# Performance work log

Measured on AMD Instinct MI355X. Metric: run time of the kernel, lower is better.

The kernel has to match this reference:

```python
import jax, jax.numpy as jnp
import numpy as np

N_EMBD = 768
HEAD_SIZE = 72
SEQ_LEN = 512
BATCH = 64

def setup_inputs() -> dict:
    key = jax.random.key(0)
    kx, kk, kq, kv = jax.random.split(key, 4)
    # Linear weights stored as [in, out] for x @ W; torch Linear init ~ U(-1/sqrt(in), 1/sqrt(in))
    bound = 1.0 / np.sqrt(N_EMBD)
    x = jax.random.normal(kx, (BATCH, SEQ_LEN, N_EMBD), dtype=jnp.float32)
    Wk = jax.random.uniform(kk, (N_EMBD, HEAD_SIZE), minval=-bound, maxval=bound, dtype=jnp.float32)
    Wq = jax.random.uniform(kq, (N_EMBD, HEAD_SIZE), minval=-bound, maxval=bound, dtype=jnp.float32)
    Wv = jax.random.uniform(kv, (N_EMBD, HEAD_SIZE), minval=-bound, maxval=bound, dtype=jnp.float32)
    return {"x": x, "Wk": Wk, "Wq": Wq, "Wv": Wv}

def reference(x, Wk, Wq, Wv):
    # Single causal self-attention head (dropout in eval mode = identity).
    k = x @ Wk  # [B, T, H]
    q = x @ Wq  # [B, T, H]
    v = x @ Wv  # [B, T, H]
    scale = k.shape[-1] ** (-0.5)
    scores = jnp.einsum('bth,bsh->bts', q, k) * scale  # [B, T, T]
    T = scores.shape[-1]
    causal = jnp.tril(jnp.ones((T, T), dtype=bool))
    scores = jnp.where(causal, scores, -jnp.inf)
    attn = jax.nn.softmax(scores, axis=-1)
    out = jnp.einsum('bts,bsh->bth', attn, v)  # [B, T, H]
    return out
```

## Files before the change

kernel.cpp:

```cpp
#include <hip/hip_runtime.h>


typedef short bf16x8 __attribute__((ext_vector_type(8)));
typedef float f32x4 __attribute__((ext_vector_type(4)));

#define DEVI __device__ __forceinline__

DEVI unsigned short f2bf(float f) {
  unsigned int u = __builtin_bit_cast(unsigned int, f);
  u = (u + 0x7fffu + ((u >> 16) & 1u)) >> 16;
  return (unsigned short)u;
}

DEVI void async16(void* lds, const void* g) {
  __builtin_amdgcn_global_load_lds(
      (const __attribute__((address_space(1))) unsigned int*)g,
      (__attribute__((address_space(3))) unsigned int*)lds, 16, 0, 0);
}

__global__ __launch_bounds__(256) void cast_x_k(const float* __restrict__ x,
                                                unsigned short* __restrict__ xb) {
  size_t i = ((size_t)blockIdx.x * 256 + threadIdx.x) * 8;
  float4 a = *(const float4*)(x + i);
  float4 c = *(const float4*)(x + i + 4);
  uint4 o;
  o.x = (unsigned)f2bf(a.x) | ((unsigned)f2bf(a.y) << 16);
  o.y = (unsigned)f2bf(a.z) | ((unsigned)f2bf(a.w) << 16);
  o.z = (unsigned)f2bf(c.x) | ((unsigned)f2bf(c.y) << 16);
  o.w = (unsigned)f2bf(c.z) | ((unsigned)f2bf(c.w) << 16);
  *(uint4*)(xb + i) = o;
}

__global__ __launch_bounds__(128) void cast_w_k(const float* __restrict__ Wk,
                                                const float* __restrict__ Wq,
                                                const float* __restrict__ Wv,
                                                unsigned short* __restrict__ wbt) {
  int mat = blockIdx.x / 80, h = blockIdx.x % 80;
  const float* W = (mat == 0) ? Wk : (mat == 1) ? Wq : Wv;
  float sc = (mat == 1) ? 0.11785113019775793f : 1.0f;
  for (int k = threadIdx.x; k < 768; k += 128) {
    float v = (h < 72) ? W[k * 72 + h] * sc : 0.0f;
    wbt[((size_t)mat * 80 + h) * 768 + k] = f2bf(v);
  }
}

struct ProjSmem {
  union {
    struct { short x[256 * 64]; short w[80 * 72]; } s;
    short t[80 * 264];
  };
};

__global__ __launch_bounds__(256, 2) void proj_k(
    const unsigned short* __restrict__ xb, const unsigned short* __restrict__ wbt,
    unsigned short* __restrict__ Kg, unsigned short* __restrict__ Qg,
    unsigned short* __restrict__ Vt) {
  __shared__ __align__(16) ProjSmem sm;
  const int mat = blockIdx.y;
  const int row0 = blockIdx.x * 256;
  const int tid = threadIdx.x, wave = tid >> 6, lane = tid & 63;
  const int quad = lane >> 4, l16 = lane & 15;

  f32x4 acc[4][5] = {};

  for (int k0 = 0; k0 < 768; k0 += 64) {
    for (int j = 0; j < 8; ++j) {
      int inst = wave * 8 + j;
      int r = inst * 8 + (lane >> 3);
      const unsigned short* g = xb + (size_t)(row0 + r) * 768 + k0 + (lane & 7) * 8;
      async16(&sm.s.x[inst * 512], g);
    }
    for (int c = tid; c < 640; c += 256) {
      int r = c >> 3, cc = (c & 7) * 8;
      uint4 d = *(const uint4*)(wbt + ((size_t)mat * 80 + r) * 768 + k0 + cc);
      *(uint4*)&sm.s.w[r * 72 + cc] = d;
    }
    __syncthreads();
    for (int ks = 0; ks < 2; ++ks) {
      bf16x8 af[4], bfr[5];
      for (int mt = 0; mt < 4; ++mt)
        af[mt] = *(const bf16x8*)&sm.s.x[(wave * 64 + mt * 16 + l16) * 64 + ks * 32 + quad * 8];
      for (int nt = 0; nt < 5; ++nt)
        bfr[nt] = *(const bf16x8*)&sm.s.w[(nt * 16 + l16) * 72 + ks * 32 + quad * 8];
      for (int mt = 0; mt < 4; ++mt)
        for (int nt = 0; nt < 5; ++nt)
          acc[mt][nt] = __builtin_amdgcn_mfma_f32_16x16x32_bf16(af[mt], bfr[nt], acc[mt][nt], 0, 0, 0);
    }
    __syncthreads();
  }

  if (mat < 2) {
    unsigned short* G = (mat == 0) ? Kg : Qg;
    for (int mt = 0; mt < 4; ++mt)
      for (int r = 0; r < 4; ++r) {
        size_t row = (size_t)row0 + wave * 64 + mt * 16 + quad * 4 + r;
        for (int nt = 0; nt < 5; ++nt)
          G[row * 96 + nt * 16 + l16] = f2bf(acc[mt][nt][r]);
        G[row * 96 + 80 + l16] = 0;
      }
  } else {
    for (int mt = 0; mt < 4; ++mt)
      for (int nt = 0; nt < 5; ++nt)
        for (int r = 0; r < 4; ++r)
          sm.t[(nt * 16 + l16) * 264 + wave * 64 + mt * 16 + quad * 4 + r] =
              (short)f2bf(acc[mt][nt][r]);
    __syncthreads();
    int b = blockIdx.x >> 1, t0 = (blockIdx.x & 1) * 256;
    for (int c = tid; c < 2560; c += 256) {
      int hr = c >> 5, tc = (c & 31) * 8;
      uint4 d = *(const uint4*)&sm.t[hr * 264 + tc];
      *(uint4*)(Vt + ((size_t)b * 80 + hr) * 512 + t0 + tc) = d;
    }
  }
}

__global__ __launch_bounds__(256, 2) void attn_k(
    const unsigned short* __restrict__ Qg, const unsigned short* __restrict__ Kg,
    const unsigned short* __restrict__ Vt, float* __restrict__ out) {
  __shared__ __align__(16) short lk[64 * 96];
  __shared__ __align__(16) short lv[80 * 64];
  __shared__ __align__(16) short lp[4][32 * 72];

  const int b = blockIdx.x >> 2, qb = blockIdx.x & 3;
  const int tid = threadIdx.x, wave = tid >> 6, lane = tid & 63;
  const int quad = lane >> 4, l16 = lane & 15;
  const int trow0 = qb * 128 + wave * 32;

  bf16x8 qf[2][3];
  for (int mt = 0; mt < 2; ++mt)
    for (int kt = 0; kt < 3; ++kt)
      qf[mt][kt] = *(const bf16x8*)(Qg + ((size_t)b * 512 + trow0 + mt * 16 + l16) * 96 +
                                    kt * 32 + quad * 8);

  f32x4 o[2][5] = {};
  float mrow[2][4], lrow[2][4];
  for (int mt = 0; mt < 2; ++mt)
    for (int r = 0; r < 4; ++r) { mrow[mt][r] = -1e30f; lrow[mt][r] = 0.0f; }

  const int nkb = 2 * qb + 2;
  for (int kb = 0; kb < nkb; ++kb) {
    const int s0 = kb * 64;
    for (int j = 0; j < 3; ++j) {
      int inst = wave * 3 + j;
      const unsigned short* g = Kg + ((size_t)b * 512 + s0) * 96 + inst * 512 + lane * 8;
      async16(&lk[inst * 512], g);
    }
    for (int j = wave; j < 10; j += 4) {
      int r = j * 8 + (lane >> 3);
      const unsigned short* g = Vt + ((size_t)b * 80 + r) * 512 + s0 + (lane & 7) * 8;
      async16(&lv[j * 512], g);
    }
    __syncthreads();

    f32x4 sacc[2][4] = {};
    for (int kt = 0; kt < 3; ++kt) {
      bf16x8 kf[4];
      for (int nt = 0; nt < 4; ++nt)
        kf[nt] = *(const bf16x8*)&lk[(nt * 16 + l16) * 96 + kt * 32 + quad * 8];
      for (int mt = 0; mt < 2; ++mt)
        for (int nt = 0; nt < 4; ++nt)
          sacc[mt][nt] = __builtin_amdgcn_mfma_f32_16x16x32_bf16(qf[mt][kt], kf[nt], sacc[mt][nt], 0, 0, 0);
    }
    if (s0 + 63 > trow0) {
      for (int mt = 0; mt < 2; ++mt)
        for (int nt = 0; nt < 4; ++nt)
          for (int r = 0; r < 4; ++r) {
            int t = trow0 + mt * 16 + quad * 4 + r;
            int ss = s0 + nt * 16 + l16;
            if (ss > t) sacc[mt][nt][r] = -1e30f;
          }
    }
    for (int mt = 0; mt < 2; ++mt)
      for (int r = 0; r < 4; ++r) {
        float mx = fmaxf(fmaxf(sacc[mt][0][r], sacc[mt][1][r]),
                         fmaxf(sacc[mt][2][r], sacc[mt][3][r]));
        for (int d = 1; d < 16; d <<= 1) mx = fmaxf(mx, __shfl_xor(mx, d, 64));
        float mold = mrow[mt][r];
        float mnew = fmaxf(mold, mx);
        float alpha = __expf(mold - mnew);
        mrow[mt][r] = mnew;
        float sum = 0.0f;
        for (int nt = 0; nt < 4; ++nt) {
          float p = __expf(sacc[mt][nt][r] - mnew);
          sacc[mt][nt][r] = p;
          sum += p;
        }
        for (int d = 1; d < 16; d <<= 1) sum += __shfl_xor(sum, d, 64);
        lrow[mt][r] = lrow[mt][r] * alpha + sum;
        for (int nt = 0; nt < 5; ++nt) o[mt][nt][r] *= alpha;
      }
    for (int mt = 0; mt < 2; ++mt)
      for (int nt = 0; nt < 4; ++nt)
        for (int r = 0; r < 4; ++r)
          lp[wave][(mt * 16 + quad * 4 + r) * 72 + nt * 16 + l16] =
              (short)f2bf(sacc[mt][nt][r]);
    for (int ks = 0; ks < 2; ++ks) {
      bf16x8 pf[2], vf[5];
      for (int mt = 0; mt < 2; ++mt)
        pf[mt] = *(const bf16x8*)&lp[wave][(mt * 16 + l16) * 72 + ks * 32 + quad * 8];
      for (int nt = 0; nt < 5; ++nt)
        vf[nt] = *(const bf16x8*)&lv[(nt * 16 + l16) * 64 + ks * 32 + quad * 8];
      for (int mt = 0; mt < 2; ++mt)
        for (int nt = 0; nt < 5; ++nt)
          o[mt][nt] = __builtin_amdgcn_mfma_f32_16x16x32_bf16(pf[mt], vf[nt], o[mt][nt], 0, 0, 0);
    }
    __syncthreads();
  }

  for (int mt = 0; mt < 2; ++mt)
    for (int r = 0; r < 4; ++r) {
      float inv = 1.0f / lrow[mt][r];
      size_t t = (size_t)b * 512 + trow0 + mt * 16 + quad * 4 + r;
      for (int nt = 0; nt < 5; ++nt) {
        int h = nt * 16 + l16;
        if (h < 72) out[t * 72 + h] = o[mt][nt][r] * inv;
      }
    }
}

extern "C" void kernel_launch(void* const* d_in, const int* in_sizes, int n_in,
                              void* d_out, int out_size, void* d_ws, size_t ws_size,
                              hipStream_t stream) {
  const float* x  = (const float*)d_in[0];
  const float* Wk = (const float*)d_in[1];
  const float* Wq = (const float*)d_in[2];
  const float* Wv = (const float*)d_in[3];
  float* out = (float*)d_out;

  char* ws = (char*)d_ws;
  unsigned short* xb  = (unsigned short*)(ws);
  unsigned short* Kg  = (unsigned short*)(ws + 50331648);
  unsigned short* Qg  = (unsigned short*)(ws + 56623104);
  unsigned short* Vt  = (unsigned short*)(ws + 62914560);
  unsigned short* wbt = (unsigned short*)(ws + 68157440);

  cast_x_k<<<12288, 256, 0, stream>>>(x, xb);
  cast_w_k<<<240, 128, 0, stream>>>(Wk, Wq, Wv, wbt);
  proj_k<<<dim3(128, 3), 256, 0, stream>>>(xb, wbt, Kg, Qg, Vt);
  attn_k<<<256, 256, 0, stream>>>(Qg, Kg, Vt, out);
}
```

Before: 224.1 us.

## Halve proj and attention tiles, balance causal blocks, fold row-sum into PV MFMA

The projection kernel now uses 128-row tiles, doubling the grid and allowing four blocks per CU. The attention kernel uses 64-query blocks with one 16-row strip per wave. It pairs heavy and light causal blocks in launch order and skips fully masked diagonal K tiles. The softmax row sum is now produced by the PV MFMA through a column of ones written into the padded V row 72, which removes the sum shuffles. This adds more K/V reloads per query row and smaller MFMA tiles per wave.

```diff
diff --git a/kernel.cpp b/kernel.cpp
--- a/kernel.cpp
+++ b/kernel.cpp
@@ -46,26 +46,26 @@
 
 struct ProjSmem {
   union {
-    struct { short x[256 * 64]; short w[80 * 72]; } s;
-    short t[80 * 264];
+    struct { short x[128 * 64]; short w[80 * 72]; } s;
+    short t[80 * 136];
   };
 };
 
-__global__ __launch_bounds__(256, 2) void proj_k(
+__global__ __launch_bounds__(256, 4) void proj_k(
     const unsigned short* __restrict__ xb, const unsigned short* __restrict__ wbt,
     unsigned short* __restrict__ Kg, unsigned short* __restrict__ Qg,
     unsigned short* __restrict__ Vt) {
   __shared__ __align__(16) ProjSmem sm;
   const int mat = blockIdx.y;
-  const int row0 = blockIdx.x * 256;
+  const int row0 = blockIdx.x * 128;
   const int tid = threadIdx.x, wave = tid >> 6, lane = tid & 63;
   const int quad = lane >> 4, l16 = lane & 15;
 
-  f32x4 acc[4][5] = {};
+  f32x4 acc[2][5] = {};
 
   for (int k0 = 0; k0 < 768; k0 += 64) {
-    for (int j = 0; j < 8; ++j) {
-      int inst = wave * 8 + j;
+    for (int j = 0; j < 4; ++j) {
+      int inst = wave * 4 + j;
       int r = inst * 8 + (lane >> 3);
       const unsigned short* g = xb + (size_t)(row0 + r) * 768 + k0 + (lane & 7) * 8;
       async16(&sm.s.x[inst * 512], g);
@@ -77,12 +77,12 @@
     }
     __syncthreads();
     for (int ks = 0; ks < 2; ++ks) {
-      bf16x8 af[4], bfr[5];
-      for (int mt = 0; mt < 4; ++mt)
-        af[mt] = *(const bf16x8*)&sm.s.x[(wave * 64 + mt * 16 + l16) * 64 + ks * 32 + quad * 8];
+      bf16x8 af[2], bfr[5];
+      for (int mt = 0; mt < 2; ++mt)
+        af[mt] = *(const bf16x8*)&sm.s.x[(wave * 32 + mt * 16 + l16) * 64 + ks * 32 + quad * 8];
       for (int nt = 0; nt < 5; ++nt)
         bfr[nt] = *(const bf16x8*)&sm.s.w[(nt * 16 + l16) * 72 + ks * 32 + quad * 8];
-      for (int mt = 0; mt < 4; ++mt)
+      for (int mt = 0; mt < 2; ++mt)
         for (int nt = 0; nt < 5; ++nt)
           acc[mt][nt] = __builtin_amdgcn_mfma_f32_16x16x32_bf16(af[mt], bfr[nt], acc[mt][nt], 0, 0, 0);
     }
@@ -91,131 +91,120 @@
 
   if (mat < 2) {
     unsigned short* G = (mat == 0) ? Kg : Qg;
-    for (int mt = 0; mt < 4; ++mt)
+    for (int mt = 0; mt < 2; ++mt)
       for (int r = 0; r < 4; ++r) {
-        size_t row = (size_t)row0 + wave * 64 + mt * 16 + quad * 4 + r;
+        size_t row = (size_t)row0 + wave * 32 + mt * 16 + quad * 4 + r;
         for (int nt = 0; nt < 5; ++nt)
           G[row * 96 + nt * 16 + l16] = f2bf(acc[mt][nt][r]);
         G[row * 96 + 80 + l16] = 0;
       }
   } else {
-    for (int mt = 0; mt < 4; ++mt)
+    for (int mt = 0; mt < 2; ++mt)
       for (int nt = 0; nt < 5; ++nt)
         for (int r = 0; r < 4; ++r)
-          sm.t[(nt * 16 + l16) * 264 + wave * 64 + mt * 16 + quad * 4 + r] =
+          sm.t[(nt * 16 + l16) * 136 + wave * 32 + mt * 16 + quad * 4 + r] =
               (short)f2bf(acc[mt][nt][r]);
     __syncthreads();
-    int b = blockIdx.x >> 1, t0 = (blockIdx.x & 1) * 256;
-    for (int c = tid; c < 2560; c += 256) {
-      int hr = c >> 5, tc = (c & 31) * 8;
-      uint4 d = *(const uint4*)&sm.t[hr * 264 + tc];
+    int b = blockIdx.x >> 2, t0 = (blockIdx.x & 3) * 128;
+    const uint4 ones = {0x3F803F80u, 0x3F803F80u, 0x3F803F80u, 0x3F803F80u};
+    for (int c = tid; c < 1280; c += 256) {
+      int hr = c >> 4, tc = (c & 15) * 8;
+      uint4 d = *(const uint4*)&sm.t[hr * 136 + tc];
+      if (hr == 72) d = ones;
       *(uint4*)(Vt + ((size_t)b * 80 + hr) * 512 + t0 + tc) = d;
     }
   }
 }
 
-__global__ __launch_bounds__(256, 2) void attn_k(
+__global__ __launch_bounds__(256, 4) void attn_k(
     const unsigned short* __restrict__ Qg, const unsigned short* __restrict__ Kg,
     const unsigned short* __restrict__ Vt, float* __restrict__ out) {
   __shared__ __align__(16) short lk[64 * 96];
   __shared__ __align__(16) short lv[80 * 64];
-  __shared__ __align__(16) short lp[4][32 * 72];
-
-  const int b = blockIdx.x >> 2, qb = blockIdx.x & 3;
+  __shared__ __align__(16) short lp[4][16 * 72];
+
+  int idx = (blockIdx.x < 256) ? blockIdx.x : 767 - blockIdx.x;
+  const int qb = 7 - (idx >> 6), b = idx & 63;
   const int tid = threadIdx.x, wave = tid >> 6, lane = tid & 63;
   const int quad = lane >> 4, l16 = lane & 15;
-  const int trow0 = qb * 128 + wave * 32;
-
-  bf16x8 qf[2][3];
-  for (int mt = 0; mt < 2; ++mt)
-    for (int kt = 0; kt < 3; ++kt)
-      qf[mt][kt] = *(const bf16x8*)(Qg + ((size_t)b * 512 + trow0 + mt * 16 + l16) * 96 +
-                                    kt * 32 + quad * 8);
-
-  f32x4 o[2][5] = {};
-  float mrow[2][4], lrow[2][4];
-  for (int mt = 0; mt < 2; ++mt)
-    for (int r = 0; r < 4; ++r) { mrow[mt][r] = -1e30f; lrow[mt][r] = 0.0f; }
-
-  const int nkb = 2 * qb + 2;
-  for (int kb = 0; kb < nkb; ++kb) {
+  const int trow0 = qb * 64 + wave * 16;
+
+  bf16x8 qf[3];
+  for (int kt = 0; kt < 3; ++kt)
+    qf[kt] = *(const bf16x8*)(Qg + ((size_t)b * 512 + trow0 + l16) * 96 + kt * 32 + quad * 8);
+
+  f32x4 o[5] = {};
+  float mrow[4];
+  for (int r = 0; r < 4; ++r) mrow[r] = -1e30f;
+
+  for (int kb = 0; kb <= qb; ++kb) {
     const int s0 = kb * 64;
+    const bool diag = (kb == qb);
+    const int nact = diag ? (wave + 1) : 4;
+
     for (int j = 0; j < 3; ++j) {
       int inst = wave * 3 + j;
-      const unsigned short* g = Kg + ((size_t)b * 512 + s0) * 96 + inst * 512 + lane * 8;
-      async16(&lk[inst * 512], g);
+      async16(&lk[inst * 512],
+              Kg + ((size_t)b * 512 + s0) * 96 + inst * 512 + lane * 8);
     }
     for (int j = wave; j < 10; j += 4) {
       int r = j * 8 + (lane >> 3);
-      const unsigned short* g = Vt + ((size_t)b * 80 + r) * 512 + s0 + (lane & 7) * 8;
-      async16(&lv[j * 512], g);
-    }
-    __syncthreads();
-
-    f32x4 sacc[2][4] = {};
+      async16(&lv[j * 512],
+              Vt + ((size_t)b * 80 + r) * 512 + s0 + (lane & 7) * 8);
+    }
+    __syncthreads();
+
+    f32x4 sacc[4];
+    for (int nt = 0; nt < 4; ++nt)
+      sacc[nt] = (diag && nt > wave) ? f32x4{-1e30f, -1e30f, -1e30f, -1e30f}
+                                     : f32x4{0.f, 0.f, 0.f, 0.f};
     for (int kt = 0; kt < 3; ++kt) {
-      bf16x8 kf[4];
+      for (int nt = 0; nt < nact; ++nt) {
+        bf16x8 kf = *(const bf16x8*)&lk[(nt * 16 + l16) * 96 + kt * 32 + quad * 8];
+        sacc[nt] = __builtin_amdgcn_mfma_f32_16x16x32_bf16(qf[kt], kf, sacc[nt], 0, 0, 0);
+      }
+    }
+    if (diag) {
+      int nt = wave;
+      for (int r = 0; r < 4; ++r) {
+        int t = trow0 + quad * 4 + r;
+        int ss = s0 + nt * 16 + l16;
+        if (ss > t) sacc[nt][r] = -1e30f;
+      }
+    }
+    for (int r = 0; r < 4; ++r) {
+      float mx = sacc[0][r];
+      for (int nt = 1; nt < nact; ++nt) mx = fmaxf(mx, sacc[nt][r]);
+      for (int d = 1; d < 16; d <<= 1) mx = fmaxf(mx, __shfl_xor(mx, d, 64));
+      float mnew = fmaxf(mrow[r], mx);
+      float alpha = __expf(mrow[r] - mnew);
+      mrow[r] = mnew;
       for (int nt = 0; nt < 4; ++nt)
-        kf[nt] = *(const bf16x8*)&lk[(nt * 16 + l16) * 96 + kt * 32 + quad * 8];
-      for (int mt = 0; mt < 2; ++mt)
-        for (int nt = 0; nt < 4; ++nt)
-          sacc[mt][nt] = __builtin_amdgcn_mfma_f32_16x16x32_bf16(qf[mt][kt], kf[nt], sacc[mt][nt], 0, 0, 0);
-    }
-    if (s0 + 63 > trow0) {
-      for (int mt = 0; mt < 2; ++mt)
-        for (int nt = 0; nt < 4; ++nt)
-          for (int r = 0; r < 4; ++r) {
-            int t = trow0 + mt * 16 + quad * 4 + r;
-            int ss = s0 + nt * 16 + l16;
-            if (ss > t) sacc[mt][nt][r] = -1e30f;
-          }
-    }
-    for (int mt = 0; mt < 2; ++mt)
-      for (int r = 0; r < 4; ++r) {
-        float mx = fmaxf(fmaxf(sacc[mt][0][r], sacc[mt][1][r]),
-                         fmaxf(sacc[mt][2][r], sacc[mt][3][r]));
-        for (int d = 1; d < 16; d <<= 1) mx = fmaxf(mx, __shfl_xor(mx, d, 64));
-        float mold = mrow[mt][r];
-        float mnew = fmaxf(mold, mx);
-        float alpha = __expf(mold - mnew);
-        mrow[mt][r] = mnew;
-        float sum = 0.0f;
-        for (int nt = 0; nt < 4; ++nt) {
-          float p = __expf(sacc[mt][nt][r] - mnew);
-          sacc[mt][nt][r] = p;
-          sum += p;
-        }
-        for (int d = 1; d < 16; d <<= 1) sum += __shfl_xor(sum, d, 64);
-        lrow[mt][r] = lrow[mt][r] * alpha + sum;
-        for (int nt = 0; nt < 5; ++nt) o[mt][nt][r] *= alpha;
-      }
-    for (int mt = 0; mt < 2; ++mt)
-      for (int nt = 0; nt < 4; ++nt)
-        for (int r = 0; r < 4; ++r)
-          lp[wave][(mt * 16 + quad * 4 + r) * 72 + nt * 16 + l16] =
-              (short)f2bf(sacc[mt][nt][r]);
+        sacc[nt][r] = (nt < nact) ? __expf(sacc[nt][r] - mnew) : 0.0f;
+      for (int nt = 0; nt < 5; ++nt) o[nt][r] *= alpha;
+    }
+    for (int nt = 0; nt < 4; ++nt)
+      for (int r = 0; r < 4; ++r)
+        lp[wave][(quad * 4 + r) * 72 + nt * 16 + l16] = (short)f2bf(sacc[nt][r]);
     for (int ks = 0; ks < 2; ++ks) {
-      bf16x8 pf[2], vf[5];
-      for (int mt = 0; mt < 2; ++mt)
-        pf[mt] = *(const bf16x8*)&lp[wave][(mt * 16 + l16) * 72 + ks * 32 + quad * 8];
-      for (int nt = 0; nt < 5; ++nt)
-        vf[nt] = *(const bf16x8*)&lv[(nt * 16 + l16) * 64 + ks * 32 + quad * 8];
-      for (int mt = 0; mt < 2; ++mt)
-        for (int nt = 0; nt < 5; ++nt)
-          o[mt][nt] = __builtin_amdgcn_mfma_f32_16x16x32_bf16(pf[mt], vf[nt], o[mt][nt], 0, 0, 0);
-    }
-    __syncthreads();
-  }
-
-  for (int mt = 0; mt < 2; ++mt)
-    for (int r = 0; r < 4; ++r) {
-      float inv = 1.0f / lrow[mt][r];
-      size_t t = (size_t)b * 512 + trow0 + mt * 16 + quad * 4 + r;
+      bf16x8 pf = *(const bf16x8*)&lp[wave][l16 * 72 + ks * 32 + quad * 8];
       for (int nt = 0; nt < 5; ++nt) {
-        int h = nt * 16 + l16;
-        if (h < 72) out[t * 72 + h] = o[mt][nt][r] * inv;
-      }
-    }
+        bf16x8 vf = *(const bf16x8*)&lv[(nt * 16 + l16) * 64 + ks * 32 + quad * 8];
+        o[nt] = __builtin_amdgcn_mfma_f32_16x16x32_bf16(pf, vf, o[nt], 0, 0, 0);
+      }
+    }
+    __syncthreads();
+  }
+
+  for (int r = 0; r < 4; ++r) {
+    float l = __shfl(o[4][r], (lane & 48) | 8, 64);
+    float inv = 1.0f / l;
+    size_t t = (size_t)b * 512 + trow0 + quad * 4 + r;
+    for (int nt = 0; nt < 5; ++nt) {
+      int h = nt * 16 + l16;
+      if (h < 72) out[t * 72 + h] = o[nt][r] * inv;
+    }
+  }
 }
 
 extern "C" void kernel_launch(void* const* d_in, const int* in_sizes, int n_in,
@@ -236,6 +225,6 @@
 
   cast_x_k<<<12288, 256, 0, stream>>>(x, xb);
   cast_w_k<<<240, 128, 0, stream>>>(Wk, Wq, Wv, wbt);
-  proj_k<<<dim3(128, 3), 256, 0, stream>>>(xb, wbt, Kg, Qg, Vt);
-  attn_k<<<256, 256, 0, stream>>>(Qg, Kg, Vt, out);
-}
+  proj_k<<<dim3(256, 3), 256, 0, stream>>>(xb, wbt, Kg, Qg, Vt);
+  attn_k<<<512, 256, 0, stream>>>(Qg, Kg, Vt, out);
+}
```

Result: faster. 218.5 us (-2.5%).
